# Optimization experiments

Measured on AMD Instinct MI355X. Metric: run time of the kernel, lower is better.

The kernel has to match this reference:

```python
import math
import jax, jax.numpy as jnp
from jax import lax
import numpy as np

SIGMA_SCALES = [0.6 * 2 ** i for i in range(6)]  # [0.6, 1.2, 2.4, 4.8, 9.6, 19.2]


def _gauss1d(sigma: float, ks: int) -> np.ndarray:
    # ax = arange(-ks//2+1, ks//2+1) for odd ks == arange(ks) - ks//2 (symmetric)
    ax = np.arange(ks, dtype=np.float32) - ks // 2
    k = np.exp(-(ax ** 2) / (2.0 * sigma ** 2))
    return (k / k.sum()).astype(np.float32)


def _kernel_size(sigma: float) -> int:
    return max(7, 2 * math.ceil(3.0 * sigma) + 1)


def _gaussian_blur(img, sigma):
    # Separable depthwise Gaussian: the torch module's 2D kernel
    # exp(-(x^2+y^2)/2s^2)/Z factors exactly into outer(g1, g1) of normalized 1D kernels.
    B, C, H, W = img.shape
    ks = _kernel_size(sigma)
    p = ks // 2
    g1 = jnp.asarray(_gauss1d(sigma, ks), dtype=img.dtype)
    x = jnp.pad(img, ((0, 0), (0, 0), (p, p), (p, p)), mode='reflect')
    kh = jnp.broadcast_to(g1.reshape(1, 1, ks, 1), (C, 1, ks, 1))
    kw = jnp.broadcast_to(g1.reshape(1, 1, 1, ks), (C, 1, 1, ks))
    dn = ('NCHW', 'OIHW', 'NCHW')
    x = lax.conv_general_dilated(x, kh, (1, 1), 'VALID', dimension_numbers=dn,
                                 feature_group_count=C)
    x = lax.conv_general_dilated(x, kw, (1, 1), 'VALID', dimension_numbers=dn,
                                 feature_group_count=C)
    return x  # (B, C, H, W)


def setup_inputs() -> dict:
    key = jax.random.key(0)
    img = jax.random.normal(key, (8, 3, 512, 512), dtype=jnp.float32)
    return {"img": img}


def reference(img) -> jnp.ndarray:
    # gaussians = [img, G(s0)*img, G(s1)*img, ...]; each scale filters the ORIGINAL img.
    gaussians = [img]
    for sigma in SIGMA_SCALES:
        gaussians.append(_gaussian_blur(img, sigma))
    n = len(gaussians)
    subbands = [gaussians[i + 1] - gaussians[i] for i in range(n - 1)]
    subbands.append(gaussians[-1])
    return jnp.stack(subbands, axis=1)  # (B, len(scales)+1, C, H, W)
```

## Files before the change

### kernel.cpp

```cpp
#include <hip/hip_runtime.h>
#include <cmath>
#include <cstddef>

#define BATCH 8
#define CH    3
#define HH    512
#define WW    512
#define NSLOT 7
#define HWX   (HH*WW)

__device__ __host__ __forceinline__ int refl(int i, int n) {
    i = i < 0 ? -i : i;
    return i >= n ? 2 * n - 2 - i : i;
}

constexpr double cexp_(double x) {
    double r = x / 64.0, term = 1.0, s = 1.0;
    for (int i = 1; i < 26; ++i) { term *= r / i; s += term; }
    for (int j = 0; j < 6; ++j) s *= s;
    return s;
}

template<int KSE> struct WArr { float w[KSE + 16]; };

template<int KSE, int KS>
constexpr WArr<KSE> make_wz(double sg) {
    WArr<KSE> a{};
    double tmp[KS] = {};
    double sum = 0.0;
    for (int t = 0; t < KS; ++t) {
        const double ax = (double)(t - KS / 2);
        tmp[t] = cexp_(-(ax * ax) / (2.0 * sg * sg));
        sum += tmp[t];
    }
    for (int i = 0; i < KSE + 16; ++i) a.w[i] = 0.0f;
    constexpr int Z = KSE - KS;
    for (int t = 0; t < KS; ++t) a.w[8 + Z + t] = (float)(tmp[t] / sum);
    return a;
}

__device__ constexpr WArr<8>   CW0 = make_wz<8,   7>(0.6);
__device__ constexpr WArr<9>   CW1 = make_wz<9,   9>(1.2);
__device__ constexpr WArr<17>  CW2 = make_wz<17, 17>(2.4);
__device__ constexpr WArr<32>  CW3 = make_wz<32, 31>(4.8);
__device__ constexpr WArr<62>  CW4 = make_wz<62, 59>(9.6);
__device__ constexpr WArr<119> CW5 = make_wz<119,117>(19.2);

template<int KS> struct VWArr {
    static constexpr int TPAD = (KS + 30) & ~15;
    float w[TPAD + 16];
};

template<int KS>
constexpr VWArr<KS> make_vw(double sg) {
    VWArr<KS> a{};
    double tmp[KS] = {};
    double sum = 0.0;
    for (int t = 0; t < KS; ++t) {
        const double ax = (double)(t - KS / 2);
        tmp[t] = cexp_(-(ax * ax) / (2.0 * sg * sg));
        sum += tmp[t];
    }
    for (int i = 0; i < VWArr<KS>::TPAD + 16; ++i) a.w[i] = 0.0f;
    for (int t = 0; t < KS; ++t) a.w[16 + t] = (float)(tmp[t] / sum);
    return a;
}

__device__ constexpr VWArr<7>   VW0 = make_vw<7>(0.6);
__device__ constexpr VWArr<9>   VW1 = make_vw<9>(1.2);
__device__ constexpr VWArr<17>  VW2 = make_vw<17>(2.4);
__device__ constexpr VWArr<31>  VW3 = make_vw<31>(4.8);
__device__ constexpr VWArr<59>  VW4 = make_vw<59>(9.6);
__device__ constexpr VWArr<117> VW5 = make_vw<117>(19.2);

template<int KS, int PD>
__device__ __forceinline__ void vpass16(const float4* __restrict__ img4,
                                        float4* __restrict__ dst,
                                        int xt, int y0, const float* __restrict__ vw)
{
    constexpr int TPAD = (KS + 30) & ~15;
    float4 acc[16];
#pragma unroll
    for (int j = 0; j < 16; ++j) acc[j] = make_float4(0.f, 0.f, 0.f, 0.f);

    float ww[16];
#pragma unroll
    for (int m = 0; m < 16; ++m) ww[m] = vw[m];

#pragma unroll 1
    for (int tb = 0; tb < TPAD; tb += 16) {
        float wn[16];
#pragma unroll
        for (int k = 0; k < 16; ++k) wn[k] = vw[tb + 16 + k];
#pragma unroll
        for (int k = 0; k < 16; ++k) {
            const int yi = refl(y0 - PD + tb + k, HH);
            const float4 v = img4[(size_t)yi * (WW / 4) + xt];
#pragma unroll
            for (int j = 0; j < 16; ++j) {
                const int mi = 16 + k - j;
                const float wt = (mi < 16) ? ww[mi] : wn[mi - 16];
                acc[j].x = fmaf(wt, v.x, acc[j].x);
                acc[j].y = fmaf(wt, v.y, acc[j].y);
                acc[j].z = fmaf(wt, v.z, acc[j].z);
                acc[j].w = fmaf(wt, v.w, acc[j].w);
            }
        }
#pragma unroll
        for (int m = 0; m < 16; ++m) ww[m] = wn[m];
    }
#pragma unroll
    for (int j = 0; j < 16; ++j) dst[(size_t)(y0 + j) * (WW / 4) + xt] = acc[j];
}

__global__ __launch_bounds__(128) void vpass6_kernel(const float* __restrict__ img,
                                                     float* __restrict__ out)
{
    const int n   = blockIdx.x;
    const int xcd = n & 7;
    const int k   = n >> 3;
    const int bcg = k / 192;
    const int rem = k - bcg * 192;
    const int s   = rem >> 5;
    const int y0  = (rem & 31) << 4;
    const int bc  = bcg * 8 + xcd;
    const int xt  = threadIdx.x;
    const int b = bc / CH, c = bc - b * CH;
    const float4* img4 = (const float4*)img + (size_t)bc * (HWX / 4);
    float4* dst = (float4*)out + ((size_t)((b * NSLOT + s + 1) * CH) + c) * (HWX / 4);
    switch (s) {
        case 0: vpass16<  7,  3>(img4, dst, xt, y0, VW0.w); break;
        case 1: vpass16<  9,  4>(img4, dst, xt, y0, VW1.w); break;
        case 2: vpass16< 17,  8>(img4, dst, xt, y0, VW2.w); break;
        case 3: vpass16< 31, 15>(img4, dst, xt, y0, VW3.w); break;
        case 4: vpass16< 59, 29>(img4, dst, xt, y0, VW4.w); break;
        default:vpass16<117, 58>(img4, dst, xt, y0, VW5.w); break;
    }
}

template<int KSE>
__device__ __forceinline__ float4 hblur6(const float* __restrict__ lrow, int xt,
                                         const WArr<KSE>& W)
{
    constexpr int NT = (KSE + 3) & ~3;
    constexpr int G  = NT / 4;
    constexpr int NR = G + 2;
    const float4* l4 = (const float4*)lrow;
    float cb[24];
#pragma unroll
    for (int s = 0; s < (NR < 4 ? NR : 4); ++s) {
        const float4 t = l4[xt + s];
        cb[(s % 6) * 4 + 0] = t.x; cb[(s % 6) * 4 + 1] = t.y;
        cb[(s % 6) * 4 + 2] = t.z; cb[(s % 6) * 4 + 3] = t.w;
    }
    float a[4] = {0.f, 0.f, 0.f, 0.f};
#pragma unroll
    for (int g = 0; g < G; ++g) {
        if (g + 4 < NR) {
            const int sl = (g + 4) % 6;
            const float4 t = l4[xt + g + 4];
            cb[sl * 4 + 0] = t.x; cb[sl * 4 + 1] = t.y;
            cb[sl * 4 + 2] = t.z; cb[sl * 4 + 3] = t.w;
        }
#pragma unroll
        for (int tt = 0; tt < 4; ++tt) {
            const float wt = W.w[8 + 4 * g + tt];
#pragma unroll
            for (int j = 0; j < 4; ++j) {
                const int q    = tt + j;
                const int slot = (g + (q >> 2)) % 6;
                a[j] = fmaf(wt, cb[slot * 4 + (q & 3)], a[j]);
            }
        }
    }
    return make_float4(a[0], a[1], a[2], a[3]);
}

#define LDSROW 3352

template<int OFF, int LEN, int PDA>
__device__ __forceinline__ void stage_row(float* __restrict__ L,
                                          const float* __restrict__ g, int xt)
{
    ((float4*)(L + OFF + PDA))[xt] = ((const float4*)g)[xt];
    if (xt < PDA) L[OFF + xt] = g[PDA - xt];
    for (int i = PDA + 512 + xt; i < LEN; i += 128)
        L[OFF + i] = g[1022 - (i - PDA)];
}

__device__ __forceinline__ float4 f4sub(float4 a, float4 b) {
    return make_float4(a.x - b.x, a.y - b.y, a.z - b.z, a.w - b.w);
}

__global__ __launch_bounds__(128) void hdiff6_kernel(const float* __restrict__ img,
                                                     float* __restrict__ out)
{
    __shared__ __align__(16) float L[LDSROW];
    const int n   = blockIdx.x;
    const int xcd = n & 7;
    const int k   = n >> 3;
    const int bcg = k >> 9;
    const int y   = k & 511;
    const int bc  = bcg * 8 + xcd;
    const int xt  = threadIdx.x;
    const int b = bc / CH, c = bc - b * CH;

    const size_t rowoff = (size_t)y * WW;
    const float4 gp0 = ((const float4*)(img + (size_t)bc * HWX + rowoff))[xt];

    constexpr size_t SSTR = (size_t)CH * HWX;
    const float* g1 = out + ((size_t)((b * NSLOT + 1) * CH) + c) * HWX + rowoff;
    stage_row<   0, 524,  4>(L, g1,            xt);
    stage_row< 524, 528,  4>(L, g1 + 1 * SSTR, xt);
    stage_row<1052, 536,  8>(L, g1 + 2 * SSTR, xt);
    stage_row<1588, 548, 16>(L, g1 + 3 * SSTR, xt);
    stage_row<2136, 580, 32>(L, g1 + 4 * SSTR, xt);
    stage_row<2716, 636, 60>(L, g1 + 5 * SSTR, xt);
    __syncthreads();

    float4* out4 = (float4*)out;
    const size_t pbase = (size_t)y * (WW / 4) + xt;
#define OSL(s) (out4 + ((size_t)((b * NSLOT + (s)) * CH) + c) * (HWX / 4) + pbase)

    float4 gp = gp0;
    float4 g;
    g = hblur6<  8>(L +    0, xt, CW0); *OSL(0) = f4sub(g, gp); gp = g;
    g = hblur6<  9>(L +  524, xt, CW1); *OSL(1) = f4sub(g, gp); gp = g;
    g = hblur6< 17>(L + 1052, xt, CW2); *OSL(2) = f4sub(g, gp); gp = g;
    g = hblur6< 32>(L + 1588, xt, CW3); *OSL(3) = f4sub(g, gp); gp = g;
    g = hblur6< 62>(L + 2136, xt, CW4); *OSL(4) = f4sub(g, gp); gp = g;
    g = hblur6<119>(L + 2716, xt, CW5); *OSL(5) = f4sub(g, gp);
    *OSL(6) = g;
#undef OSL
}

extern "C" void kernel_launch(void* const* d_in, const int* in_sizes, int n_in,
                              void* d_out, int out_size, void* d_ws, size_t ws_size,
                              hipStream_t stream) {
    const float* img = (const float*)d_in[0];
    float* out = (float*)d_out;

    hipLaunchKernelGGL(vpass6_kernel, dim3(4608), dim3(128), 0, stream, img, out);

    hipLaunchKernelGGL(hdiff6_kernel, dim3(12288), dim3(128), 0, stream, img, out);
}
```

Measured before the change: 366.9 us.

## Fuse vertical and horizontal blur passes into one kernel with LDS rows

Replaces the separate vertical-pass kernel, which wrote six intermediate planes to the output buffer, and the horizontal/difference kernel with a single kernel. Each block computes two output rows: it streams 119 input rows, accumulates all six vertical blurs in registers, and stages the results plus reflected halos in LDS for the horizontal pass and the differences. This removes the global round trip of the intermediates and one launch. In exchange, input rows are re-read many times across blocks (each row pair reads 119 rows), the fully unrolled tap loop adds code size and register pressure, and there are fewer output rows per block.

```diff
diff --git a/kernel.cpp b/kernel.cpp
--- a/kernel.cpp
+++ b/kernel.cpp
@@ -46,14 +46,11 @@
 __device__ constexpr WArr<62>  CW4 = make_wz<62, 59>(9.6);
 __device__ constexpr WArr<119> CW5 = make_wz<119,117>(19.2);
 
-template<int KS> struct VWArr {
-    static constexpr int TPAD = (KS + 30) & ~15;
-    float w[TPAD + 16];
-};
+template<int KS> struct CVArr { float w[KS]; };
 
 template<int KS>
-constexpr VWArr<KS> make_vw(double sg) {
-    VWArr<KS> a{};
+constexpr CVArr<KS> make_cv(double sg) {
+    CVArr<KS> a{};
     double tmp[KS] = {};
     double sum = 0.0;
     for (int t = 0; t < KS; ++t) {
@@ -61,85 +58,19 @@
         tmp[t] = cexp_(-(ax * ax) / (2.0 * sg * sg));
         sum += tmp[t];
     }
-    for (int i = 0; i < VWArr<KS>::TPAD + 16; ++i) a.w[i] = 0.0f;
-    for (int t = 0; t < KS; ++t) a.w[16 + t] = (float)(tmp[t] / sum);
+    for (int t = 0; t < KS; ++t) a.w[t] = (float)(tmp[t] / sum);
     return a;
 }
 
-__device__ constexpr VWArr<7>   VW0 = make_vw<7>(0.6);
-__device__ constexpr VWArr<9>   VW1 = make_vw<9>(1.2);
-__device__ constexpr VWArr<17>  VW2 = make_vw<17>(2.4);
-__device__ constexpr VWArr<31>  VW3 = make_vw<31>(4.8);
-__device__ constexpr VWArr<59>  VW4 = make_vw<59>(9.6);
-__device__ constexpr VWArr<117> VW5 = make_vw<117>(19.2);
-
-template<int KS, int PD>
-__device__ __forceinline__ void vpass16(const float4* __restrict__ img4,
-                                        float4* __restrict__ dst,
-                                        int xt, int y0, const float* __restrict__ vw)
-{
-    constexpr int TPAD = (KS + 30) & ~15;
-    float4 acc[16];
-#pragma unroll
-    for (int j = 0; j < 16; ++j) acc[j] = make_float4(0.f, 0.f, 0.f, 0.f);
-
-    float ww[16];
-#pragma unroll
-    for (int m = 0; m < 16; ++m) ww[m] = vw[m];
-
-#pragma unroll 1
-    for (int tb = 0; tb < TPAD; tb += 16) {
-        float wn[16];
-#pragma unroll
-        for (int k = 0; k < 16; ++k) wn[k] = vw[tb + 16 + k];
-#pragma unroll
-        for (int k = 0; k < 16; ++k) {
-            const int yi = refl(y0 - PD + tb + k, HH);
-            const float4 v = img4[(size_t)yi * (WW / 4) + xt];
-#pragma unroll
-            for (int j = 0; j < 16; ++j) {
-                const int mi = 16 + k - j;
-                const float wt = (mi < 16) ? ww[mi] : wn[mi - 16];
-                acc[j].x = fmaf(wt, v.x, acc[j].x);
-                acc[j].y = fmaf(wt, v.y, acc[j].y);
-                acc[j].z = fmaf(wt, v.z, acc[j].z);
-                acc[j].w = fmaf(wt, v.w, acc[j].w);
-            }
-        }
-#pragma unroll
-        for (int m = 0; m < 16; ++m) ww[m] = wn[m];
-    }
-#pragma unroll
-    for (int j = 0; j < 16; ++j) dst[(size_t)(y0 + j) * (WW / 4) + xt] = acc[j];
-}
-
-__global__ __launch_bounds__(128) void vpass6_kernel(const float* __restrict__ img,
-                                                     float* __restrict__ out)
-{
-    const int n   = blockIdx.x;
-    const int xcd = n & 7;
-    const int k   = n >> 3;
-    const int bcg = k / 192;
-    const int rem = k - bcg * 192;
-    const int s   = rem >> 5;
-    const int y0  = (rem & 31) << 4;
-    const int bc  = bcg * 8 + xcd;
-    const int xt  = threadIdx.x;
-    const int b = bc / CH, c = bc - b * CH;
-    const float4* img4 = (const float4*)img + (size_t)bc * (HWX / 4);
-    float4* dst = (float4*)out + ((size_t)((b * NSLOT + s + 1) * CH) + c) * (HWX / 4);
-    switch (s) {
-        case 0: vpass16<  7,  3>(img4, dst, xt, y0, VW0.w); break;
-        case 1: vpass16<  9,  4>(img4, dst, xt, y0, VW1.w); break;
-        case 2: vpass16< 17,  8>(img4, dst, xt, y0, VW2.w); break;
-        case 3: vpass16< 31, 15>(img4, dst, xt, y0, VW3.w); break;
-        case 4: vpass16< 59, 29>(img4, dst, xt, y0, VW4.w); break;
-        default:vpass16<117, 58>(img4, dst, xt, y0, VW5.w); break;
-    }
-}
+__device__ constexpr CVArr<7>   CV0 = make_cv<7>(0.6);
+__device__ constexpr CVArr<9>   CV1 = make_cv<9>(1.2);
+__device__ constexpr CVArr<17>  CV2 = make_cv<17>(2.4);
+__device__ constexpr CVArr<31>  CV3 = make_cv<31>(4.8);
+__device__ constexpr CVArr<59>  CV4 = make_cv<59>(9.6);
+__device__ constexpr CVArr<117> CV5 = make_cv<117>(19.2);
 
 template<int KSE>
-__device__ __forceinline__ float4 hblur6(const float* __restrict__ lrow, int xt,
+__device__ __forceinline__ float4 hblur4(const float* __restrict__ lrow, int xt,
                                          const WArr<KSE>& W)
 {
     constexpr int NT = (KSE + 3) & ~3;
@@ -178,60 +109,114 @@
 
 #define LDSROW 3352
 
-template<int OFF, int LEN, int PDA>
-__device__ __forceinline__ void stage_row(float* __restrict__ L,
-                                          const float* __restrict__ g, int xt)
-{
-    ((float4*)(L + OFF + PDA))[xt] = ((const float4*)g)[xt];
-    if (xt < PDA) L[OFF + xt] = g[PDA - xt];
-    for (int i = PDA + 512 + xt; i < LEN; i += 128)
-        L[OFF + i] = g[1022 - (i - PDA)];
-}
-
 __device__ __forceinline__ float4 f4sub(float4 a, float4 b) {
     return make_float4(a.x - b.x, a.y - b.y, a.z - b.z, a.w - b.w);
 }
 
-__global__ __launch_bounds__(128) void hdiff6_kernel(const float* __restrict__ img,
-                                                     float* __restrict__ out)
+#define VTAP(s, KS, PD, W)                                                     \
+    {                                                                          \
+        const int i = t - (58 - PD) - j;                                       \
+        if (i >= 0 && i < KS) {                                                \
+            const float wt = W.w[i];                \
+            acc[j][s][0] = fmaf(wt, v.x, acc[j][s][0]);                        \
+            acc[j][s][1] = fmaf(wt, v.y, acc[j][s][1]);                        \
+            acc[j][s][2] = fmaf(wt, v.z, acc[j][s][2]);                        \
+            acc[j][s][3] = fmaf(wt, v.w, acc[j][s][3]);                        \
+        }                                                                      \
+    }
+
+#define HALO(OFF, LEN, PDA)                                                    \
+    {                                                                          \
+        for (int i2 = u; i2 < PDA; i2 += 64)                                   \
+            Lx[OFF + i2] = Lx[OFF + 2 * PDA - i2];                             \
+        for (int i2 = PDA + 512 + u; i2 < LEN; i2 += 64)                       \
+            Lx[OFF + i2] = Lx[OFF + 2 * PDA + 1022 - i2];                      \
+    }
+
+__global__ __launch_bounds__(128) void fused_dog_kernel(const float* __restrict__ img,
+                                                        float* __restrict__ out)
 {
-    __shared__ __align__(16) float L[LDSROW];
+    __shared__ __align__(16) float lds[2][LDSROW];
+    const int xt  = threadIdx.x;
     const int n   = blockIdx.x;
     const int xcd = n & 7;
     const int k   = n >> 3;
-    const int bcg = k >> 9;
-    const int y   = k & 511;
+    const int bcg = k >> 8;
+    const int y   = (k & 255) * 2;
     const int bc  = bcg * 8 + xcd;
-    const int xt  = threadIdx.x;
     const int b = bc / CH, c = bc - b * CH;
 
-    const size_t rowoff = (size_t)y * WW;
-    const float4 gp0 = ((const float4*)(img + (size_t)bc * HWX + rowoff))[xt];
-
-    constexpr size_t SSTR = (size_t)CH * HWX;
-    const float* g1 = out + ((size_t)((b * NSLOT + 1) * CH) + c) * HWX + rowoff;
-    stage_row<   0, 524,  4>(L, g1,            xt);
-    stage_row< 524, 528,  4>(L, g1 + 1 * SSTR, xt);
-    stage_row<1052, 536,  8>(L, g1 + 2 * SSTR, xt);
-    stage_row<1588, 548, 16>(L, g1 + 3 * SSTR, xt);
-    stage_row<2136, 580, 32>(L, g1 + 4 * SSTR, xt);
-    stage_row<2716, 636, 60>(L, g1 + 5 * SSTR, xt);
+    const float* ibase = img + (size_t)bc * HWX;
+
+    float acc[2][6][4];
+#pragma unroll
+    for (int j = 0; j < 2; ++j)
+#pragma unroll
+        for (int s = 0; s < 6; ++s)
+#pragma unroll
+            for (int q = 0; q < 4; ++q) acc[j][s][q] = 0.f;
+
+    float4 g0a = make_float4(0.f, 0.f, 0.f, 0.f);
+    float4 g0b = make_float4(0.f, 0.f, 0.f, 0.f);
+
+#pragma unroll
+    for (int t = 0; t < 119; ++t) {
+        const int yi = refl(y - 58 + t, HH);
+        const float4 v = ((const float4*)(ibase + (size_t)yi * WW))[xt];
+        if (t == 58) g0a = v;
+        if (t == 59) g0b = v;
+#pragma unroll
+        for (int j = 0; j < 2; ++j) {
+            VTAP(0,   7,  3, CV0)
+            VTAP(1,   9,  4, CV1)
+            VTAP(2,  17,  8, CV2)
+            VTAP(3,  31, 15, CV3)
+            VTAP(4,  59, 29, CV4)
+            VTAP(5, 117, 58, CV5)
+        }
+    }
+
+#pragma unroll
+    for (int j = 0; j < 2; ++j) {
+        float* L = lds[j];
+        ((float4*)(L +    0 +  4))[xt] = make_float4(acc[j][0][0], acc[j][0][1], acc[j][0][2], acc[j][0][3]);
+        ((float4*)(L +  524 +  4))[xt] = make_float4(acc[j][1][0], acc[j][1][1], acc[j][1][2], acc[j][1][3]);
+        ((float4*)(L + 1052 +  8))[xt] = make_float4(acc[j][2][0], acc[j][2][1], acc[j][2][2], acc[j][2][3]);
+        ((float4*)(L + 1588 + 16))[xt] = make_float4(acc[j][3][0], acc[j][3][1], acc[j][3][2], acc[j][3][3]);
+        ((float4*)(L + 2136 + 32))[xt] = make_float4(acc[j][4][0], acc[j][4][1], acc[j][4][2], acc[j][4][3]);
+        ((float4*)(L + 2716 + 60))[xt] = make_float4(acc[j][5][0], acc[j][5][1], acc[j][5][2], acc[j][5][3]);
+    }
     __syncthreads();
 
+    {
+        const int u = xt & 63;
+        float* Lx = lds[xt >> 6];
+        HALO(   0, 524,  4)
+        HALO( 524, 528,  4)
+        HALO(1052, 536,  8)
+        HALO(1588, 548, 16)
+        HALO(2136, 580, 32)
+        HALO(2716, 636, 60)
+    }
+    __syncthreads();
+
     float4* out4 = (float4*)out;
-    const size_t pbase = (size_t)y * (WW / 4) + xt;
+#pragma unroll 1
+    for (int j = 0; j < 2; ++j) {
+        const float* L = lds[j];
+        const size_t pbase = (size_t)(y + j) * (WW / 4) + xt;
 #define OSL(s) (out4 + ((size_t)((b * NSLOT + (s)) * CH) + c) * (HWX / 4) + pbase)
-
-    float4 gp = gp0;
-    float4 g;
-    g = hblur6<  8>(L +    0, xt, CW0); *OSL(0) = f4sub(g, gp); gp = g;
-    g = hblur6<  9>(L +  524, xt, CW1); *OSL(1) = f4sub(g, gp); gp = g;
-    g = hblur6< 17>(L + 1052, xt, CW2); *OSL(2) = f4sub(g, gp); gp = g;
-    g = hblur6< 32>(L + 1588, xt, CW3); *OSL(3) = f4sub(g, gp); gp = g;
-    g = hblur6< 62>(L + 2136, xt, CW4); *OSL(4) = f4sub(g, gp); gp = g;
-    g = hblur6<119>(L + 2716, xt, CW5); *OSL(5) = f4sub(g, gp);
-    *OSL(6) = g;
+        float4 gp = j ? g0b : g0a;
+        float4 g;
+        g = hblur4<  8>(L +    0, xt, CW0); *OSL(0) = f4sub(g, gp); gp = g;
+        g = hblur4<  9>(L +  524, xt, CW1); *OSL(1) = f4sub(g, gp); gp = g;
+        g = hblur4< 17>(L + 1052, xt, CW2); *OSL(2) = f4sub(g, gp); gp = g;
+        g = hblur4< 32>(L + 1588, xt, CW3); *OSL(3) = f4sub(g, gp); gp = g;
+        g = hblur4< 62>(L + 2136, xt, CW4); *OSL(4) = f4sub(g, gp); gp = g;
+        g = hblur4<119>(L + 2716, xt, CW5); *OSL(5) = f4sub(g, gp);
+        *OSL(6) = g;
 #undef OSL
+    }
 }
 
 extern "C" void kernel_launch(void* const* d_in, const int* in_sizes, int n_in,
@@ -239,8 +224,5 @@
                               hipStream_t stream) {
     const float* img = (const float*)d_in[0];
     float* out = (float*)d_out;
-
-    hipLaunchKernelGGL(vpass6_kernel, dim3(4608), dim3(128), 0, stream, img, out);
-
-    hipLaunchKernelGGL(hdiff6_kernel, dim3(12288), dim3(128), 0, stream, img, out);
-}
+    hipLaunchKernelGGL(fused_dog_kernel, dim3(6144), dim3(128), 0, stream, img, out);
+}
```

Measured after the change: 697.4 us. 1.9x slower.
